# Kernel tuning notes

Measured on AMD Instinct MI355X. Metric: run time of the kernel, lower is better.

Reference implementation:

```python
import jax, jax.numpy as jnp
import numpy as np


def setup_inputs() -> dict:
    key = jax.random.key(0)
    k1, k2, k3, k4 = jax.random.split(key, 4)
    B, V, NB, C, K, O = 2, 50000, 16, 64, 8, 64
    x = jax.random.normal(k1, (B, V, C), dtype=jnp.float32)
    # adj: 1-based neighbor indices, 0 == NULL (points at the zero pad row)
    adj = jax.random.randint(k2, (V, NB), 0, V + 1, dtype=jnp.int32)
    u = jax.random.normal(k3, (C, K), dtype=jnp.float32) * 0.05
    W = jax.random.normal(k4, (C, K * O), dtype=jnp.float32) * 0.05
    return {"x": x, "u": u, "W": W, "adj": adj}


def reference(x, u, W, adj):
    B, V, C = x.shape
    NB = adj.shape[1]
    K = u.shape[1]
    O = W.shape[1] // K

    # pad with zero row at index 0, gather neighbor patches: [B, V, NB, C]
    xp = jnp.concatenate([jnp.zeros((B, 1, C), x.dtype), x], axis=1)
    patches = xp[:, adj]

    # translation-invariant attention logits: (x_i - x_j) u, masked at NULL
    mask = (adj != 0)[None, :, :, None]            # [1, V, NB, 1]
    diff = jnp.where(mask, x[:, :, None, :] - patches, jnp.zeros((), x.dtype))
    q = jax.nn.softmax(jnp.einsum('bvnc,ck->bvnk', diff, u), axis=-1)  # softmax over kernel dim

    # per-vertex 1/deg (0 for isolated vertices)
    deg = jnp.sum(adj != 0, axis=-1).astype(x.dtype)   # [V]
    inv_deg = jnp.where(deg > 0, 1.0 / deg, jnp.zeros((), x.dtype))

    # fused (patches @ W) * q summed over neighbors and kernels -> [B, V, O]
    Wr = W.reshape(C, K, O)
    out = jnp.einsum('bvnc,cko,bvnk->bvo', patches, Wr, q)
    return out * inv_deg[None, :, None]
```

## Files before the change

kernel.cpp:

```cpp
#include <hip/hip_runtime.h>
#include <hip/hip_bf16.h>


constexpr int BB = 2;
constexpr int VV = 50000;
#define NB 16
#define CC 64
#define KK 8
#define OO 64
#define TV 32

typedef __attribute__((ext_vector_type(8))) short bf16x8;
typedef __attribute__((ext_vector_type(4))) float f32x4;

static __device__ __forceinline__ short f2b(float f) {
    __hip_bfloat16 h = __float2bfloat16(f);
    return *reinterpret_cast<short*>(&h);
}

__global__ void xu_kernel(const float* __restrict__ x,
                          const float* __restrict__ u,
                          float* __restrict__ xu, int total) {
    int t = blockIdx.x * blockDim.x + threadIdx.x;
    if (t >= total) return;
    const float4* xr = reinterpret_cast<const float4*>(x + (size_t)t * CC);
    float acc[KK];
#pragma unroll
    for (int k = 0; k < KK; ++k) acc[k] = 0.f;
#pragma unroll
    for (int c4 = 0; c4 < CC / 4; ++c4) {
        float4 xv = xr[c4];
#pragma unroll
        for (int k = 0; k < KK; ++k) {
            acc[k] = fmaf(xv.x, u[(c4 * 4 + 0) * KK + k], acc[k]);
            acc[k] = fmaf(xv.y, u[(c4 * 4 + 1) * KK + k], acc[k]);
            acc[k] = fmaf(xv.z, u[(c4 * 4 + 2) * KK + k], acc[k]);
            acc[k] = fmaf(xv.w, u[(c4 * 4 + 3) * KK + k], acc[k]);
        }
    }
    float4* xo = reinterpret_cast<float4*>(xu + (size_t)t * KK);
    xo[0] = make_float4(acc[0], acc[1], acc[2], acc[3]);
    xo[1] = make_float4(acc[4], acc[5], acc[6], acc[7]);
}

__global__ void wprep_kernel(const float* __restrict__ W,
                             short* __restrict__ Wb) {
    int dst = blockIdx.x * blockDim.x + threadIdx.x;
    int e = dst & 7;
    int l = (dst >> 3) & 63;
    int ctk = dst >> 9;
    int gct = ctk & 3;
    int ks = ctk >> 2;
    int ck = ks * 32 + (l >> 4) * 8 + e;
    int o = gct * 16 + (l & 15);
    Wb[dst] = f2b(W[ck * OO + o]);
}

__global__ __launch_bounds__(256, 3) void feast_fused(
    const float* __restrict__ x, const int* __restrict__ adj,
    const float* __restrict__ xu, const short* __restrict__ Wb,
    float* __restrict__ out) {
    __shared__ short Mlds[TV * 512];
    __shared__ float sInvd[TV];

    int t = threadIdx.x;
    int b = blockIdx.y;
    int v0 = blockIdx.x * TV;

    {
        int vl = t >> 3;
        int j = t & 7;
        int v = v0 + vl;
        if (v >= VV) v = VV - 1;

        int a[NB];
        const int4* arow = reinterpret_cast<const int4*>(adj + (size_t)v * NB);
#pragma unroll
        for (int n4 = 0; n4 < NB / 4; ++n4) {
            int4 t4 = arow[n4];
            a[n4 * 4 + 0] = t4.x;
            a[n4 * 4 + 1] = t4.y;
            a[n4 * 4 + 2] = t4.z;
            a[n4 * 4 + 3] = t4.w;
        }

        const float4* xu4 = reinterpret_cast<const float4*>(xu);
        const float4* x4 = reinterpret_cast<const float4*>(x);
        int gs = b * VV + v;
        float4 s0 = xu4[gs * 2 + 0], s1 = xu4[gs * 2 + 1];
        float xs[KK] = {s0.x, s0.y, s0.z, s0.w, s1.x, s1.y, s1.z, s1.w};

        float acc[8][KK];
#pragma unroll
        for (int c = 0; c < 8; ++c)
#pragma unroll
            for (int k = 0; k < KK; ++k) acc[c][k] = 0.f;
        float deg = 0.f;

#pragma unroll 4
        for (int n = 0; n < NB; ++n) {
            int an = a[n];
            bool act = (an != 0);
            deg += act ? 1.f : 0.f;
            int row = act ? (an - 1) : 0;
            int g = b * VV + row;
            float4 n0 = xu4[g * 2 + 0], n1 = xu4[g * 2 + 1];
            float l8[KK] = {xs[0] - n0.x, xs[1] - n0.y, xs[2] - n0.z,
                            xs[3] - n0.w, xs[4] - n1.x, xs[5] - n1.y,
                            xs[6] - n1.z, xs[7] - n1.w};
            float mx = l8[0];
#pragma unroll
            for (int k = 1; k < KK; ++k) mx = fmaxf(mx, l8[k]);
            float sum = 0.f;
            float e8[KK];
#pragma unroll
            for (int k = 0; k < KK; ++k) {
                e8[k] = __expf(l8[k] - mx);
                sum += e8[k];
            }
            float r = act ? (1.f / sum) : 0.f;
            float qk[KK];
#pragma unroll
            for (int k = 0; k < KK; ++k) qk[k] = e8[k] * r;
            float4 p0 = x4[(size_t)g * 16 + j * 2 + 0];
            float4 p1 = x4[(size_t)g * 16 + j * 2 + 1];
            float p[8] = {p0.x, p0.y, p0.z, p0.w, p1.x, p1.y, p1.z, p1.w};
#pragma unroll
            for (int c = 0; c < 8; ++c)
#pragma unroll
                for (int k = 0; k < KK; ++k)
                    acc[c][k] = fmaf(p[c], qk[k], acc[c][k]);
        }

        if (j == 0) sInvd[vl] = (deg > 0.f) ? (1.f / deg) : 0.f;

#pragma unroll
        for (int s = 0; s < 8; ++s) {
            bf16x8 w;
#pragma unroll
            for (int k = 0; k < KK; ++k) w[k] = f2b(acc[s][k]);
            int slot = (j * 8 + s) ^ (vl & 7);
            *reinterpret_cast<bf16x8*>(
                reinterpret_cast<char*>(Mlds) + vl * 1024 + slot * 16) = w;
        }
    }
    __syncthreads();

    {
        int wid = t >> 6;
        int l = t & 63;
        int rt = wid >> 1;
        int ch = wid & 1;
        int r = rt * 16 + (l & 15);

        f32x4 acc2[2];
        acc2[0] = (f32x4){0.f, 0.f, 0.f, 0.f};
        acc2[1] = (f32x4){0.f, 0.f, 0.f, 0.f};
        const bf16x8* WbV = reinterpret_cast<const bf16x8*>(Wb);

#pragma unroll
        for (int ks = 0; ks < 16; ++ks) {
            int slotA = (ks * 4 + (l >> 4)) ^ (r & 7);
            bf16x8 afrag = *reinterpret_cast<const bf16x8*>(
                reinterpret_cast<const char*>(Mlds) + r * 1024 + slotA * 16);
#pragma unroll
            for (int ct = 0; ct < 2; ++ct) {
                int gct = ch * 2 + ct;
                bf16x8 bfrag = WbV[(ks * 4 + gct) * 64 + l];
                acc2[ct] = __builtin_amdgcn_mfma_f32_16x16x32_bf16(
                    afrag, bfrag, acc2[ct], 0, 0, 0);
            }
        }

#pragma unroll
        for (int ct = 0; ct < 2; ++ct) {
            int col = ch * 32 + ct * 16 + (l & 15);
#pragma unroll
            for (int jr = 0; jr < 4; ++jr) {
                int rowl = rt * 16 + (l >> 4) * 4 + jr;
                int vv = v0 + rowl;
                if (vv < VV) {
                    out[((size_t)b * VV + vv) * OO + col] =
                        acc2[ct][jr] * sInvd[rowl];
                }
            }
        }
    }
}

extern "C" void kernel_launch(void* const* d_in, const int* in_sizes, int n_in,
                              void* d_out, int out_size, void* d_ws,
                              size_t ws_size, hipStream_t stream) {
    const float* x = (const float*)d_in[0];
    const float* u = (const float*)d_in[1];
    const float* W = (const float*)d_in[2];
    const int* adj = (const int*)d_in[3];
    float* out = (float*)d_out;

    float* xu = (float*)d_ws;
    short* Wb = (short*)((char*)d_ws + (size_t)BB * VV * KK * sizeof(float));

    int total = BB * VV;
    xu_kernel<<<(total + 255) / 256, 256, 0, stream>>>(x, u, xu, total);
    wprep_kernel<<<(CC * KK * OO) / 256, 256, 0, stream>>>(W, Wb);
    dim3 g((VV + TV - 1) / TV, BB);
    feast_fused<<<g, 256, 0, stream>>>(x, adj, xu, Wb, out);
}
```

Baseline: 177.6 us.

## Share softmax weights via LDS, software-pipeline neighbor gathers, merge prep kernels

The per-neighbor softmax is now computed once per (vertex, neighbor) and spread across the 8 threads of each vertex through LDS, where before all 8 threads recomputed it. The neighbor feature gathers are double-buffered, so the loads for the next pair are issued before the FMAs on the current pair. The two prep kernels are merged into one launch, the xu computation is split across two threads per row, and launch bounds are raised to 4 blocks per CU. In exchange there are extra barriers and more register pressure, and the LDS swizzle changes.

```diff
diff --git a/kernel.cpp b/kernel.cpp
--- a/kernel.cpp
+++ b/kernel.cpp
@@ -18,131 +18,182 @@
     return *reinterpret_cast<short*>(&h);
 }
 
-__global__ void xu_kernel(const float* __restrict__ x,
-                          const float* __restrict__ u,
-                          float* __restrict__ xu, int total) {
-    int t = blockIdx.x * blockDim.x + threadIdx.x;
-    if (t >= total) return;
-    const float4* xr = reinterpret_cast<const float4*>(x + (size_t)t * CC);
-    float acc[KK];
-#pragma unroll
-    for (int k = 0; k < KK; ++k) acc[k] = 0.f;
-#pragma unroll
-    for (int c4 = 0; c4 < CC / 4; ++c4) {
-        float4 xv = xr[c4];
-#pragma unroll
-        for (int k = 0; k < KK; ++k) {
-            acc[k] = fmaf(xv.x, u[(c4 * 4 + 0) * KK + k], acc[k]);
-            acc[k] = fmaf(xv.y, u[(c4 * 4 + 1) * KK + k], acc[k]);
-            acc[k] = fmaf(xv.z, u[(c4 * 4 + 2) * KK + k], acc[k]);
-            acc[k] = fmaf(xv.w, u[(c4 * 4 + 3) * KK + k], acc[k]);
+constexpr int XUB = (BB * VV * 2 + 255) / 256;
+constexpr int WPB = (CC * KK * OO) / 256;
+
+__global__ void prep_kernel(const float* __restrict__ x,
+                            const float* __restrict__ u,
+                            float* __restrict__ xu,
+                            const float* __restrict__ W,
+                            short* __restrict__ Wb) {
+    int blk = blockIdx.x;
+    if (blk < XUB) {
+        int t = blk * 256 + threadIdx.x;
+        if (t >= BB * VV * 2) return;
+        int g = t >> 1, half = t & 1;
+        const float4* xr =
+            reinterpret_cast<const float4*>(x) + (size_t)g * (CC / 4);
+        const float4* u4 = reinterpret_cast<const float4*>(u);
+        float a0 = 0.f, a1 = 0.f, a2 = 0.f, a3 = 0.f;
+#pragma unroll
+        for (int c4 = 0; c4 < CC / 4; ++c4) {
+            float4 xv = xr[c4];
+            float4 u0 = u4[(c4 * 4 + 0) * 2 + half];
+            float4 u1 = u4[(c4 * 4 + 1) * 2 + half];
+            float4 u2 = u4[(c4 * 4 + 2) * 2 + half];
+            float4 u3 = u4[(c4 * 4 + 3) * 2 + half];
+            a0 = fmaf(xv.x, u0.x, a0); a1 = fmaf(xv.x, u0.y, a1);
+            a2 = fmaf(xv.x, u0.z, a2); a3 = fmaf(xv.x, u0.w, a3);
+            a0 = fmaf(xv.y, u1.x, a0); a1 = fmaf(xv.y, u1.y, a1);
+            a2 = fmaf(xv.y, u1.z, a2); a3 = fmaf(xv.y, u1.w, a3);
+            a0 = fmaf(xv.z, u2.x, a0); a1 = fmaf(xv.z, u2.y, a1);
+            a2 = fmaf(xv.z, u2.z, a2); a3 = fmaf(xv.z, u2.w, a3);
+            a0 = fmaf(xv.w, u3.x, a0); a1 = fmaf(xv.w, u3.y, a1);
+            a2 = fmaf(xv.w, u3.z, a2); a3 = fmaf(xv.w, u3.w, a3);
         }
-    }
-    float4* xo = reinterpret_cast<float4*>(xu + (size_t)t * KK);
-    xo[0] = make_float4(acc[0], acc[1], acc[2], acc[3]);
-    xo[1] = make_float4(acc[4], acc[5], acc[6], acc[7]);
-}
-
-__global__ void wprep_kernel(const float* __restrict__ W,
-                             short* __restrict__ Wb) {
-    int dst = blockIdx.x * blockDim.x + threadIdx.x;
-    int e = dst & 7;
-    int l = (dst >> 3) & 63;
-    int ctk = dst >> 9;
-    int gct = ctk & 3;
-    int ks = ctk >> 2;
-    int ck = ks * 32 + (l >> 4) * 8 + e;
-    int o = gct * 16 + (l & 15);
-    Wb[dst] = f2b(W[ck * OO + o]);
-}
-
-__global__ __launch_bounds__(256, 3) void feast_fused(
+        reinterpret_cast<float4*>(xu)[(size_t)g * 2 + half] =
+            make_float4(a0, a1, a2, a3);
+    } else {
+        int dst = (blk - XUB) * 256 + threadIdx.x;
+        int e = dst & 7;
+        int l = (dst >> 3) & 63;
+        int ctk = dst >> 9;
+        int gct = ctk & 3;
+        int ks = ctk >> 2;
+        int ck = ks * 32 + (l >> 4) * 8 + e;
+        int o = gct * 16 + (l & 15);
+        Wb[dst] = f2b(W[ck * OO + o]);
+    }
+}
+
+__global__ __launch_bounds__(256, 4) void feast_fused(
     const float* __restrict__ x, const int* __restrict__ adj,
     const float* __restrict__ xu, const short* __restrict__ Wb,
     float* __restrict__ out) {
-    __shared__ short Mlds[TV * 512];
+    __shared__ char smem[TV * 1024];
     __shared__ float sInvd[TV];
 
     int t = threadIdx.x;
     int b = blockIdx.y;
     int v0 = blockIdx.x * TV;
+    int vl = t >> 3;
+    int j = t & 7;
+    int v = v0 + vl;
+    if (v >= VV) v = VV - 1;
+
+    float* qlds = reinterpret_cast<float*>(smem);
+
+    int a[NB];
+    const int4* arow = reinterpret_cast<const int4*>(adj + (size_t)v * NB);
+#pragma unroll
+    for (int n4 = 0; n4 < 4; ++n4) {
+        int4 t4 = arow[n4];
+        a[n4 * 4 + 0] = t4.x;
+        a[n4 * 4 + 1] = t4.y;
+        a[n4 * 4 + 2] = t4.z;
+        a[n4 * 4 + 3] = t4.w;
+    }
+    float deg = 0.f;
+#pragma unroll
+    for (int n = 0; n < NB; ++n) deg += (a[n] != 0) ? 1.f : 0.f;
+    if (j == 0) sInvd[vl] = (deg > 0.f) ? (1.f / deg) : 0.f;
+
+    const float4* xu4 = reinterpret_cast<const float4*>(xu);
+    const float4* x4 = reinterpret_cast<const float4*>(x);
 
     {
-        int vl = t >> 3;
-        int j = t & 7;
-        int v = v0 + vl;
-        if (v >= VV) v = VV - 1;
-
-        int a[NB];
-        const int4* arow = reinterpret_cast<const int4*>(adj + (size_t)v * NB);
-#pragma unroll
-        for (int n4 = 0; n4 < NB / 4; ++n4) {
-            int4 t4 = arow[n4];
-            a[n4 * 4 + 0] = t4.x;
-            a[n4 * 4 + 1] = t4.y;
-            a[n4 * 4 + 2] = t4.z;
-            a[n4 * 4 + 3] = t4.w;
-        }
-
-        const float4* xu4 = reinterpret_cast<const float4*>(xu);
-        const float4* x4 = reinterpret_cast<const float4*>(x);
         int gs = b * VV + v;
-        float4 s0 = xu4[gs * 2 + 0], s1 = xu4[gs * 2 + 1];
+        float4 s0 = xu4[(size_t)gs * 2], s1 = xu4[(size_t)gs * 2 + 1];
         float xs[KK] = {s0.x, s0.y, s0.z, s0.w, s1.x, s1.y, s1.z, s1.w};
-
-        float acc[8][KK];
-#pragma unroll
-        for (int c = 0; c < 8; ++c)
-#pragma unroll
-            for (int k = 0; k < KK; ++k) acc[c][k] = 0.f;
-        float deg = 0.f;
-
-#pragma unroll 4
-        for (int n = 0; n < NB; ++n) {
-            int an = a[n];
-            bool act = (an != 0);
-            deg += act ? 1.f : 0.f;
-            int row = act ? (an - 1) : 0;
-            int g = b * VV + row;
-            float4 n0 = xu4[g * 2 + 0], n1 = xu4[g * 2 + 1];
+        int2 ap = *reinterpret_cast<const int2*>(adj + (size_t)v * NB + 2 * j);
+
+        auto qbuild = [&](int an, int nn) {
+            int g = b * VV + (an ? an - 1 : 0);
+            float4 n0 = xu4[(size_t)g * 2], n1 = xu4[(size_t)g * 2 + 1];
             float l8[KK] = {xs[0] - n0.x, xs[1] - n0.y, xs[2] - n0.z,
                             xs[3] - n0.w, xs[4] - n1.x, xs[5] - n1.y,
                             xs[6] - n1.z, xs[7] - n1.w};
             float mx = l8[0];
 #pragma unroll
             for (int k = 1; k < KK; ++k) mx = fmaxf(mx, l8[k]);
+            float e8[KK];
             float sum = 0.f;
-            float e8[KK];
 #pragma unroll
             for (int k = 0; k < KK; ++k) {
                 e8[k] = __expf(l8[k] - mx);
                 sum += e8[k];
             }
-            float r = act ? (1.f / sum) : 0.f;
-            float qk[KK];
-#pragma unroll
-            for (int k = 0; k < KK; ++k) qk[k] = e8[k] * r;
-            float4 p0 = x4[(size_t)g * 16 + j * 2 + 0];
-            float4 p1 = x4[(size_t)g * 16 + j * 2 + 1];
-            float p[8] = {p0.x, p0.y, p0.z, p0.w, p1.x, p1.y, p1.z, p1.w};
-#pragma unroll
-            for (int c = 0; c < 8; ++c)
-#pragma unroll
-                for (int k = 0; k < KK; ++k)
-                    acc[c][k] = fmaf(p[c], qk[k], acc[c][k]);
-        }
-
-        if (j == 0) sInvd[vl] = (deg > 0.f) ? (1.f / deg) : 0.f;
-
-#pragma unroll
-        for (int s = 0; s < 8; ++s) {
-            bf16x8 w;
-#pragma unroll
-            for (int k = 0; k < KK; ++k) w[k] = f2b(acc[s][k]);
-            int slot = (j * 8 + s) ^ (vl & 7);
-            *reinterpret_cast<bf16x8*>(
-                reinterpret_cast<char*>(Mlds) + vl * 1024 + slot * 16) = w;
-        }
+            float r = an ? (1.f / sum) : 0.f;
+            f32x4 q0 = {e8[0] * r, e8[1] * r, e8[2] * r, e8[3] * r};
+            f32x4 q1 = {e8[4] * r, e8[5] * r, e8[6] * r, e8[7] * r};
+            f32x4* qp = reinterpret_cast<f32x4*>(qlds + nn * 256 + vl * 8);
+            qp[0] = q0;
+            qp[1] = q1;
+        };
+        qbuild(ap.x, 2 * j);
+        qbuild(ap.y, 2 * j + 1);
+    }
+
+#define GOFF(n) (((size_t)(b * VV + (a[n] ? a[n] - 1 : 0))) * 16 + j * 2)
+#define CONS(n, P0, P1)                                                        \
+    {                                                                          \
+        const f32x4* qv =                                                      \
+            reinterpret_cast<const f32x4*>(qlds + (n) * 256 + vl * 8);         \
+        f32x4 q0 = qv[0];                                                      \
+        f32x4 q1 = qv[1];                                                      \
+        float p[8] = {P0.x, P0.y, P0.z, P0.w, P1.x, P1.y, P1.z, P1.w};         \
+        _Pragma("unroll") for (int c = 0; c < 8; ++c) {                        \
+            _Pragma("unroll") for (int k = 0; k < 4; ++k) {                    \
+                acc[c][k] = fmaf(p[c], q0[k], acc[c][k]);                      \
+                acc[c][k + 4] = fmaf(p[c], q1[k], acc[c][k + 4]);              \
+            }                                                                  \
+        }                                                                      \
+    }
+#define LOADPAIR(n, D0, D1, D2, D3)                                            \
+    {                                                                          \
+        size_t g0 = GOFF(n), g1 = GOFF((n) + 1);                               \
+        D0 = x4[g0];                                                           \
+        D1 = x4[g0 + 1];                                                       \
+        D2 = x4[g1];                                                           \
+        D3 = x4[g1 + 1];                                                       \
+    }
+
+    float4 A0, A1, A2, A3, B0, B1, B2, B3;
+    LOADPAIR(0, A0, A1, A2, A3)
+    __syncthreads();
+
+    float acc[8][KK];
+#pragma unroll
+    for (int c = 0; c < 8; ++c)
+#pragma unroll
+        for (int k = 0; k < KK; ++k) acc[c][k] = 0.f;
+
+    LOADPAIR(2, B0, B1, B2, B3)
+    CONS(0, A0, A1) CONS(1, A2, A3)
+    LOADPAIR(4, A0, A1, A2, A3)
+    CONS(2, B0, B1) CONS(3, B2, B3)
+    LOADPAIR(6, B0, B1, B2, B3)
+    CONS(4, A0, A1) CONS(5, A2, A3)
+    LOADPAIR(8, A0, A1, A2, A3)
+    CONS(6, B0, B1) CONS(7, B2, B3)
+    LOADPAIR(10, B0, B1, B2, B3)
+    CONS(8, A0, A1) CONS(9, A2, A3)
+    LOADPAIR(12, A0, A1, A2, A3)
+    CONS(10, B0, B1) CONS(11, B2, B3)
+    LOADPAIR(14, B0, B1, B2, B3)
+    CONS(12, A0, A1) CONS(13, A2, A3)
+    CONS(14, B0, B1) CONS(15, B2, B3)
+
+    __syncthreads();
+
+#pragma unroll
+    for (int s = 0; s < 8; ++s) {
+        bf16x8 w;
+#pragma unroll
+        for (int k = 0; k < KK; ++k) w[k] = f2b(acc[s][k]);
+        int slot = j * 8 + s;
+        int slot2 = slot ^ j ^ (vl & 7);
+        *reinterpret_cast<bf16x8*>(smem + vl * 1024 + slot2 * 16) = w;
     }
     __syncthreads();
 
@@ -160,13 +211,13 @@
 
 #pragma unroll
         for (int ks = 0; ks < 16; ++ks) {
-            int slotA = (ks * 4 + (l >> 4)) ^ (r & 7);
+            int ks4h = ks * 4 + (l >> 4);
+            int slotA = ks4h ^ ((ks4h >> 3) & 7) ^ (r & 7);
             bf16x8 afrag = *reinterpret_cast<const bf16x8*>(
-                reinterpret_cast<const char*>(Mlds) + r * 1024 + slotA * 16);
+                smem + r * 1024 + slotA * 16);
 #pragma unroll
             for (int ct = 0; ct < 2; ++ct) {
-                int gct = ch * 2 + ct;
-                bf16x8 bfrag = WbV[(ks * 4 + gct) * 64 + l];
+                bf16x8 bfrag = WbV[(ks * 4 + ch * 2 + ct) * 64 + l];
                 acc2[ct] = __builtin_amdgcn_mfma_f32_16x16x32_bf16(
                     afrag, bfrag, acc2[ct], 0, 0, 0);
             }
@@ -200,9 +251,7 @@
     float* xu = (float*)d_ws;
     short* Wb = (short*)((char*)d_ws + (size_t)BB * VV * KK * sizeof(float));
 
-    int total = BB * VV;
-    xu_kernel<<<(total + 255) / 256, 256, 0, stream>>>(x, u, xu, total);
-    wprep_kernel<<<(CC * KK * OO) / 256, 256, 0, stream>>>(W, Wb);
+    prep_kernel<<<XUB + WPB, 256, 0, stream>>>(x, u, xu, W, Wb);
     dim3 g((VV + TV - 1) / TV, BB);
     feast_fused<<<g, 256, 0, stream>>>(x, adj, xu, Wb, out);
 }
```

Result: slower. 435.9 us (+145.5%).
